# Optimization experiments

Measured on AMD Instinct MI355X. Metric: run time of the kernel, lower is better.

Reference implementation:

```python
import jax, jax.numpy as jnp
import numpy as np

P = 8  # patch_shape (8, 8) -> per-window sequence length 64


def _bias_indices():
    # pairs of (i, j) coords inside an 8x8 patch window
    pairs = np.array([[i, j] for i in range(P) for j in range(P)])  # [64, 2]
    rel = pairs[:, None, :] - pairs[None, :, :] + P - 1  # [64, 64, 2] in [0, 14]
    return rel[:, :, 0], rel[:, :, 1]


def _make_mask(Wy, Wx):
    # generate_mask with apply_shift=True, patch_shape=(8,8)
    s = P // 2
    m = np.zeros((Wy, Wx, P, P, P, P), dtype=bool)
    m[-1, :, :s, :, s:, :] = True
    m[-1, :, s:, :, :s, :] = True
    m[:, -1, :, :s, :, s:] = True
    m[:, -1, :, s:, :, :s] = True
    return jnp.asarray(m.reshape(Wy, Wx, P * P, P * P))


def setup_inputs() -> dict:
    key = jax.random.key(0)
    ks = jax.random.split(key, 10)
    B, Wy, Wx, S, E, H, hd = 16, 16, 16, 64, 128, 4, 32
    sc = 0.05
    return {
        "patches": jax.random.normal(ks[0], (B, Wy, Wx, S, E), dtype=jnp.float32),
        "Wq": jax.random.normal(ks[1], (H, E, hd), dtype=jnp.float32) * sc,
        "bq": jax.random.normal(ks[2], (H, hd), dtype=jnp.float32) * sc,
        "Wk": jax.random.normal(ks[3], (H, E, hd), dtype=jnp.float32) * sc,
        "bk": jax.random.normal(ks[4], (H, hd), dtype=jnp.float32) * sc,
        "Wv": jax.random.normal(ks[5], (H, E, hd), dtype=jnp.float32) * sc,
        "bv": jax.random.normal(ks[6], (H, hd), dtype=jnp.float32) * sc,
        "pos_bias": jax.random.normal(ks[7], (2 * P - 1, 2 * P - 1), dtype=jnp.float32) * 0.02,
        "Wo": jax.random.normal(ks[8], (E, E), dtype=jnp.float32) * sc,
        "bo": jax.random.normal(ks[9], (E,), dtype=jnp.float32) * sc,
        "mask": _make_mask(Wy, Wx),
    }


def reference(patches, Wq, bq, Wk, bk, Wv, bv, pos_bias, Wo, bo, mask):
    hd = Wq.shape[-1]
    B, Wy, Wx, S, E = patches.shape
    H = Wq.shape[0]
    # per-head Q/K/V projections (torch loops over heads; here batched over h)
    q = jnp.einsum("bvwse,hed->bvwhsd", patches, Wq) + bq[:, None, :]
    k = jnp.einsum("bvwse,hed->bvwhsd", patches, Wk) + bk[:, None, :]
    v = jnp.einsum("bvwse,hed->bvwhsd", patches, Wv) + bv[:, None, :]
    logits = jnp.einsum("bvwhqd,bvwhkd->bvwhqk", q, k) / jnp.sqrt(jnp.asarray(hd, patches.dtype))
    ri, ci = _bias_indices()
    logits = logits + pos_bias[ri, ci]  # gather [15,15] -> [64,64]
    logits = jnp.where(mask[None, :, :, None, :, :], -jnp.inf, logits)
    attn = jax.nn.softmax(logits, axis=-1)
    out = jnp.einsum("bvwhqk,bvwhkd->bvwhqd", attn, v)
    # concat heads: [..., H, S, hd] -> [..., S, H*hd]
    out = jnp.swapaxes(out, 3, 4).reshape(B, Wy, Wx, S, H * hd)
    return jnp.einsum("bvwse,ef->bvwsf", out, Wo) + bo
```

## Files before the change

kernel.cpp:

```cpp
#include <hip/hip_runtime.h>
#include <hip/hip_bf16.h>

typedef float f32x4 __attribute__((ext_vector_type(4)));
typedef short bf16x8 __attribute__((ext_vector_type(8)));
typedef short s16x4 __attribute__((ext_vector_type(4)));
typedef unsigned int u32;

#define MFMA16(a, b, c) __builtin_amdgcn_mfma_f32_16x16x32_bf16((a), (b), (c), 0, 0, 0)

__device__ __forceinline__ unsigned short f2bf(float x) {
    union { float f; unsigned int u; } a; a.f = x;
    unsigned int r = a.u + 0x7fffu + ((a.u >> 16) & 1u);
    return (unsigned short)(r >> 16);
}

__global__ void prep_kernel(const float* __restrict__ Wq, const float* __restrict__ bq,
                            const float* __restrict__ Wk, const float* __restrict__ bk,
                            const float* __restrict__ Wv, const float* __restrict__ bv,
                            const float* __restrict__ pos_bias, const float* __restrict__ Wo,
                            unsigned short* __restrict__ WT, unsigned short* __restrict__ WoT,
                            float* __restrict__ bqkv, float* __restrict__ bm) {
    const float LOG2E = 1.4426950408889634f;
    int t = blockIdx.x * blockDim.x + threadIdx.x;
    int nt = gridDim.x * blockDim.x;
    for (int i = t; i < 384 * 128; i += nt) {
        int c = i >> 7, kk = i & 127;
        int h = c / 96, rem = c - h * 96, p = rem >> 5, n = rem & 31;
        const float* W = (p == 0) ? Wq : (p == 1 ? Wk : Wv);
        WT[i] = f2bf(W[(h * 128 + kk) * 32 + n]);
    }
    for (int i = t; i < 128 * 128; i += nt) {
        int n = i >> 7, kk = i & 127;
        WoT[i] = f2bf(Wo[kk * 128 + n]);
    }
    for (int i = t; i < 384; i += nt) {
        int h = i / 96, rem = i - h * 96, p = rem >> 5, n = rem & 31;
        const float* b = (p == 0) ? bq : (p == 1 ? bk : bv);
        bqkv[i] = b[h * 32 + n];
    }
    for (int i = t; i < 4 * 4 * 4 * 64 * 4; i += nt) {
        int r = i & 3, l = (i >> 2) & 63, kt = (i >> 8) & 3, qt = (i >> 10) & 3, v = (i >> 12) & 3;
        int q = qt * 16 + (l & 15);
        int k = kt * 16 + ((l >> 4) << 2) + r;
        int qi = q >> 3, qj = q & 7, ki = k >> 3, kj = k & 7;
        bool masked = (((v >> 1) != 0) && ((qi < 4) != (ki < 4))) ||
                      (((v & 1) != 0) && ((qj < 4) != (kj < 4)));
        bm[i] = masked ? -1e30f : pos_bias[(qi - ki + 7) * 15 + (qj - kj + 7)] * LOG2E;
    }
}

__launch_bounds__(256, 3)
__global__ void swin_kernel(const float* __restrict__ patches,
                            const unsigned short* __restrict__ WT,
                            const float* __restrict__ bqkv,
                            const float* __restrict__ bm,
                            const unsigned short* __restrict__ WoT,
                            const float* __restrict__ bo,
                            float* __restrict__ out) {
    __shared__ short lds[24576];
    const int win = blockIdx.x;
    const int wy = (win >> 4) & 15, wx = win & 15;
    const int tid = threadIdx.x;
    const int lane = tid & 63;
    const int h = tid >> 6;
    const int l15 = lane & 15, l4 = lane >> 4;
    const int sw15 = (l15 & 7) << 3;
    const f32x4 zero = {0.f, 0.f, 0.f, 0.f};

    {
        const float4* src = reinterpret_cast<const float4*>(patches + (size_t)win * 8192);
        #pragma unroll
        for (int i = 0; i < 8; ++i) {
            int idx4 = i * 256 + tid;
            float4 v = src[idx4];
            int row = idx4 >> 5;
            int col = (idx4 & 31) << 2;
            s16x4 pk;
            pk[0] = (short)f2bf(v.x); pk[1] = (short)f2bf(v.y);
            pk[2] = (short)f2bf(v.z); pk[3] = (short)f2bf(v.w);
            *reinterpret_cast<s16x4*>(&lds[row * 128 + (col ^ ((row & 7) << 3))]) = pk;
        }
    }
    __syncthreads();

    const int qkbase = 8192 + h * 4096;
    const int vbase = h * 2048;

    bf16x8 xa[4][4];
    #pragma unroll
    for (int mt = 0; mt < 4; ++mt)
        #pragma unroll
        for (int ks = 0; ks < 4; ++ks)
            xa[mt][ks] = *reinterpret_cast<const bf16x8*>(
                &lds[(mt * 16 + l15) * 128 + ((ks * 32 + l4 * 8) ^ sw15)]);

    #pragma unroll
    for (int ct = 0; ct < 4; ++ct) {
        bf16x8 wb[4];
        #pragma unroll
        for (int ks = 0; ks < 4; ++ks)
            wb[ks] = *reinterpret_cast<const bf16x8*>(
                &WT[(h * 96 + ct * 16 + l15) * 128 + ks * 32 + l4 * 8]);
        float b4[4];
        #pragma unroll
        for (int r = 0; r < 4; ++r) b4[r] = bqkv[h * 96 + ct * 16 + l4 * 4 + r];
        #pragma unroll
        for (int mt = 0; mt < 4; ++mt) {
            f32x4 a = zero;
            #pragma unroll
            for (int ks = 0; ks < 4; ++ks) a = MFMA16(wb[ks], xa[mt][ks], a);
            int tok = mt * 16 + l15;
            int cc0 = (ct * 16 + l4 * 4) ^ sw15;
            s16x4 pk;
            #pragma unroll
            for (int r = 0; r < 4; ++r) pk[r] = (short)f2bf(a[r] + b4[r]);
            *reinterpret_cast<s16x4*>(&lds[qkbase + tok * 64 + cc0]) = pk;
        }
    }
    __syncthreads();

    #pragma unroll
    for (int ctv = 0; ctv < 2; ++ctv) {
        bf16x8 wb[4];
        #pragma unroll
        for (int ks = 0; ks < 4; ++ks)
            wb[ks] = *reinterpret_cast<const bf16x8*>(
                &WT[(h * 96 + 64 + ctv * 16 + l15) * 128 + ks * 32 + l4 * 8]);
        float bb = bqkv[h * 96 + 64 + ctv * 16 + l15];
        #pragma unroll
        for (int mt = 0; mt < 4; ++mt) {
            f32x4 a = zero;
            #pragma unroll
            for (int ks = 0; ks < 4; ++ks) a = MFMA16(xa[mt][ks], wb[ks], a);
            int n = ctv * 16 + l15;
            int tok0 = (mt * 16 + l4 * 4) ^ sw15;
            s16x4 pk;
            #pragma unroll
            for (int r = 0; r < 4; ++r) pk[r] = (short)f2bf(a[r] + bb);
            *reinterpret_cast<s16x4*>(&lds[vbase + n * 64 + tok0]) = pk;
        }
    }

    bf16x8 kfrag[4], vf[2][2];
    #pragma unroll
    for (int kt = 0; kt < 4; ++kt)
        kfrag[kt] = *reinterpret_cast<const bf16x8*>(
            &lds[qkbase + (kt * 16 + l15) * 64 + ((32 + l4 * 8) ^ sw15)]);
    #pragma unroll
    for (int nt = 0; nt < 2; ++nt)
        #pragma unroll
        for (int ks = 0; ks < 2; ++ks)
            vf[nt][ks] = *reinterpret_cast<const bf16x8*>(
                &lds[vbase + (nt * 16 + l15) * 64 + ((ks * 32 + l4 * 8) ^ sw15)]);

    f32x4 O[2][4];
    #pragma unroll
    for (int nt = 0; nt < 2; ++nt)
        #pragma unroll
        for (int qt = 0; qt < 4; ++qt) O[nt][qt] = zero;

    const int mv = ((wy == 15) ? 2 : 0) + ((wx == 15) ? 1 : 0);
    const float4* bmv = reinterpret_cast<const float4*>(bm);
    const float rs2 = 0.2550348660629988f;
    const int sA = ((l4 & 1) << 5) + l15;
    const int sB = sA + 16;

    #pragma unroll
    for (int qt = 0; qt < 4; ++qt) {
        bf16x8 qfrag = *reinterpret_cast<const bf16x8*>(
            &lds[qkbase + (qt * 16 + l15) * 64 + ((l4 * 8) ^ sw15)]);
        f32x4 LT[4];
        #pragma unroll
        for (int kt = 0; kt < 4; ++kt) LT[kt] = MFMA16(kfrag[kt], qfrag, zero);

        float x[4][4];
        float m = -3.0e38f;
        #pragma unroll
        for (int kt = 0; kt < 4; ++kt) {
            float4 b4 = bmv[((mv * 4 + qt) * 4 + kt) * 64 + lane];
            x[kt][0] = LT[kt][0] * rs2 + b4.x;
            x[kt][1] = LT[kt][1] * rs2 + b4.y;
            x[kt][2] = LT[kt][2] * rs2 + b4.z;
            x[kt][3] = LT[kt][3] * rs2 + b4.w;
            m = fmaxf(m, fmaxf(fmaxf(x[kt][0], x[kt][1]), fmaxf(x[kt][2], x[kt][3])));
        }
        m = fmaxf(m, __shfl_xor(m, 16));
        m = fmaxf(m, __shfl_xor(m, 32));
        float s = 0.f;
        #pragma unroll
        for (int kt = 0; kt < 4; ++kt)
            #pragma unroll
            for (int r = 0; r < 4; ++r) {
                float e = exp2f(x[kt][r] - m);
                x[kt][r] = e;
                s += e;
            }
        s += __shfl_xor(s, 16);
        s += __shfl_xor(s, 32);
        float inv = 1.0f / s;

        u32 w[4][2];
        #pragma unroll
        for (int kt = 0; kt < 4; ++kt) {
            w[kt][0] = (u32)f2bf(x[kt][0] * inv) | ((u32)f2bf(x[kt][1] * inv) << 16);
            w[kt][1] = (u32)f2bf(x[kt][2] * inv) | ((u32)f2bf(x[kt][3] * inv) << 16);
        }
        u32 fr[2][4];
        #pragma unroll
        for (int kt = 0; kt < 4; ++kt) {
            u32 a0 = __shfl(w[kt][0], sA);
            u32 a1 = __shfl(w[kt][1], sA);
            u32 b0 = __shfl(w[kt][0], sB);
            u32 b1 = __shfl(w[kt][1], sB);
            if ((kt & 1) == (l4 >> 1)) {
                const int ks = kt >> 1;
                fr[ks][0] = a0; fr[ks][1] = a1; fr[ks][2] = b0; fr[ks][3] = b1;
            }
        }
        bf16x8 pf0, pf1;
        {
            union { u32 u[4]; bf16x8 v; } c0, c1;
            c0.u[0] = fr[0][0]; c0.u[1] = fr[0][1]; c0.u[2] = fr[0][2]; c0.u[3] = fr[0][3];
            c1.u[0] = fr[1][0]; c1.u[1] = fr[1][1]; c1.u[2] = fr[1][2]; c1.u[3] = fr[1][3];
            pf0 = c0.v; pf1 = c1.v;
        }
        #pragma unroll
        for (int nt = 0; nt < 2; ++nt) {
            O[nt][qt] = MFMA16(vf[nt][0], pf0, O[nt][qt]);
            O[nt][qt] = MFMA16(vf[nt][1], pf1, O[nt][qt]);
        }
    }
    __syncthreads();

    #pragma unroll
    for (int nt = 0; nt < 2; ++nt)
        #pragma unroll
        for (int qt = 0; qt < 4; ++qt) {
            int q = qt * 16 + l15;
            int f0 = (h * 32 + nt * 16 + l4 * 4) ^ sw15;
            s16x4 pk;
            #pragma unroll
            for (int r = 0; r < 4; ++r) pk[r] = (short)f2bf(O[nt][qt][r]);
            *reinterpret_cast<s16x4*>(&lds[8192 + q * 128 + f0]) = pk;
        }
    __syncthreads();

    {
        bf16x8 wf[2][4];
        #pragma unroll
        for (int nt = 0; nt < 2; ++nt)
            #pragma unroll
            for (int ks = 0; ks < 4; ++ks)
                wf[nt][ks] = *reinterpret_cast<const bf16x8*>(
                    &WoT[(h * 32 + nt * 16 + l15) * 128 + ks * 32 + l4 * 8]);
        float4 bo4[2];
        #pragma unroll
        for (int nt = 0; nt < 2; ++nt)
            bo4[nt] = *reinterpret_cast<const float4*>(&bo[h * 32 + nt * 16 + l4 * 4]);
        float* outw = out + (size_t)win * 8192;
        #pragma unroll
        for (int mt = 0; mt < 4; ++mt) {
            bf16x8 af[4];
            #pragma unroll
            for (int ks = 0; ks < 4; ++ks)
                af[ks] = *reinterpret_cast<const bf16x8*>(
                    &lds[8192 + (mt * 16 + l15) * 128 + ((ks * 32 + l4 * 8) ^ sw15)]);
            #pragma unroll
            for (int nt = 0; nt < 2; ++nt) {
                f32x4 a = zero;
                #pragma unroll
                for (int ks = 0; ks < 4; ++ks) a = MFMA16(wf[nt][ks], af[ks], a);
                float4 st;
                st.x = a[0] + bo4[nt].x;
                st.y = a[1] + bo4[nt].y;
                st.z = a[2] + bo4[nt].z;
                st.w = a[3] + bo4[nt].w;
                *reinterpret_cast<float4*>(
                    &outw[(size_t)(mt * 16 + l15) * 128 + h * 32 + nt * 16 + l4 * 4]) = st;
            }
        }
    }
}

extern "C" void kernel_launch(void* const* d_in, const int* in_sizes, int n_in,
                              void* d_out, int out_size, void* d_ws, size_t ws_size,
                              hipStream_t stream) {
    const float* patches  = (const float*)d_in[0];
    const float* Wq       = (const float*)d_in[1];
    const float* bq       = (const float*)d_in[2];
    const float* Wk       = (const float*)d_in[3];
    const float* bk       = (const float*)d_in[4];
    const float* Wv       = (const float*)d_in[5];
    const float* bv       = (const float*)d_in[6];
    const float* pos_bias = (const float*)d_in[7];
    const float* Wo       = (const float*)d_in[8];
    const float* bo       = (const float*)d_in[9];

    char* ws = (char*)d_ws;
    unsigned short* WT  = (unsigned short*)(ws);
    unsigned short* WoT = (unsigned short*)(ws + 98304);
    float* bqkv         = (float*)(ws + 131072);
    float* bm           = (float*)(ws + 132608);

    hipLaunchKernelGGL(prep_kernel, dim3(64), dim3(256), 0, stream,
                       Wq, bq, Wk, bk, Wv, bv, pos_bias, Wo, WT, WoT, bqkv, bm);
    hipLaunchKernelGGL(swin_kernel, dim3(4096), dim3(256), 0, stream,
                       patches, WT, bqkv, bm, WoT, bo, (float*)d_out);
}
```

Measured before the change: 110.0 us.

## Make swin kernel persistent with register prefetch of next window's patches

Turns the one-window-per-block kernel into a persistent loop over windows with a grid of 768 blocks (256 CUs × 3 blocks). The next window's fp32 patches are prefetched into registers while the current window's QKV projection and attention run, and the previous window's output projection is deferred to the start of the next iteration. It also raises wave priority around MFMA sections with s_setprio. The aim is to hide global-load latency and cut per-block launch and fill overhead, at the cost of more live registers (the px prefetch buffer) and a more complex schedule.

```diff
diff --git a/kernel.cpp b/kernel.cpp
--- a/kernel.cpp
+++ b/kernel.cpp
@@ -49,6 +49,8 @@
     }
 }
 
+#define SWIN_GRID 768
+
 __launch_bounds__(256, 3)
 __global__ void swin_kernel(const float* __restrict__ patches,
                             const unsigned short* __restrict__ WT,
@@ -58,8 +60,6 @@
                             const float* __restrict__ bo,
                             float* __restrict__ out) {
     __shared__ short lds[24576];
-    const int win = blockIdx.x;
-    const int wy = (win >> 4) & 15, wx = win & 15;
     const int tid = threadIdx.x;
     const int lane = tid & 63;
     const int h = tid >> 6;
@@ -67,183 +67,252 @@
     const int sw15 = (l15 & 7) << 3;
     const f32x4 zero = {0.f, 0.f, 0.f, 0.f};
 
+    const int qkbase = 8192 + h * 4096;
+    const int vbase = h * 2048;
+    const int sA = ((l4 & 1) << 5) + l15;
+    const int sB = sA + 16;
+    const float rs2 = 0.2550348660629988f;
+    const float4* bmv = reinterpret_cast<const float4*>(bm);
+
+    int w = blockIdx.x;
+    float4 px[8];
     {
-        const float4* src = reinterpret_cast<const float4*>(patches + (size_t)win * 8192);
+        const float4* src = reinterpret_cast<const float4*>(patches + (size_t)w * 8192);
+        #pragma unroll
+        for (int i = 0; i < 8; ++i) px[i] = src[i * 256 + tid];
+    }
+    #pragma unroll
+    for (int i = 0; i < 8; ++i) {
+        int idx4 = i * 256 + tid;
+        int row = idx4 >> 5, col = (idx4 & 31) << 2;
+        s16x4 pk;
+        pk[0] = (short)f2bf(px[i].x); pk[1] = (short)f2bf(px[i].y);
+        pk[2] = (short)f2bf(px[i].z); pk[3] = (short)f2bf(px[i].w);
+        *reinterpret_cast<s16x4*>(&lds[row * 128 + (col ^ ((row & 7) << 3))]) = pk;
+    }
+    __syncthreads();
+
+    int prev = -1;
+    for (; w < 4096; w += SWIN_GRID) {
+        if (prev >= 0) {
+            bf16x8 wf[2][4];
+            #pragma unroll
+            for (int nt = 0; nt < 2; ++nt)
+                #pragma unroll
+                for (int ks = 0; ks < 4; ++ks)
+                    wf[nt][ks] = *reinterpret_cast<const bf16x8*>(
+                        &WoT[(h * 32 + nt * 16 + l15) * 128 + ks * 32 + l4 * 8]);
+            float4 bo4[2];
+            #pragma unroll
+            for (int nt = 0; nt < 2; ++nt)
+                bo4[nt] = *reinterpret_cast<const float4*>(&bo[h * 32 + nt * 16 + l4 * 4]);
+            float* outw = out + (size_t)prev * 8192;
+            #pragma unroll
+            for (int mt = 0; mt < 4; ++mt) {
+                bf16x8 af[4];
+                #pragma unroll
+                for (int ks = 0; ks < 4; ++ks)
+                    af[ks] = *reinterpret_cast<const bf16x8*>(
+                        &lds[8192 + (mt * 16 + l15) * 128 + ((ks * 32 + l4 * 8) ^ sw15)]);
+                __builtin_amdgcn_s_setprio(1);
+                #pragma unroll
+                for (int nt = 0; nt < 2; ++nt) {
+                    f32x4 a = zero;
+                    #pragma unroll
+                    for (int ks = 0; ks < 4; ++ks) a = MFMA16(wf[nt][ks], af[ks], a);
+                    float4 st;
+                    st.x = a[0] + bo4[nt].x;
+                    st.y = a[1] + bo4[nt].y;
+                    st.z = a[2] + bo4[nt].z;
+                    st.w = a[3] + bo4[nt].w;
+                    *reinterpret_cast<float4*>(
+                        &outw[(size_t)(mt * 16 + l15) * 128 + h * 32 + nt * 16 + l4 * 4]) = st;
+                }
+                __builtin_amdgcn_s_setprio(0);
+            }
+        }
+
+        bf16x8 xa[4][4];
+        #pragma unroll
+        for (int mt = 0; mt < 4; ++mt)
+            #pragma unroll
+            for (int ks = 0; ks < 4; ++ks)
+                xa[mt][ks] = *reinterpret_cast<const bf16x8*>(
+                    &lds[(mt * 16 + l15) * 128 + ((ks * 32 + l4 * 8) ^ sw15)]);
+        __syncthreads();
+
+        {
+            int wn = w + SWIN_GRID;
+            const float4* srcn = reinterpret_cast<const float4*>(
+                patches + (size_t)(wn < 4096 ? wn : w) * 8192);
+            #pragma unroll
+            for (int i = 0; i < 8; ++i) px[i] = srcn[i * 256 + tid];
+        }
+
+        #pragma unroll
+        for (int ct = 0; ct < 4; ++ct) {
+            bf16x8 wb[4];
+            #pragma unroll
+            for (int ks = 0; ks < 4; ++ks)
+                wb[ks] = *reinterpret_cast<const bf16x8*>(
+                    &WT[(h * 96 + ct * 16 + l15) * 128 + ks * 32 + l4 * 8]);
+            float b4[4];
+            #pragma unroll
+            for (int r = 0; r < 4; ++r) b4[r] = bqkv[h * 96 + ct * 16 + l4 * 4 + r];
+            __builtin_amdgcn_s_setprio(1);
+            #pragma unroll
+            for (int mt = 0; mt < 4; ++mt) {
+                f32x4 a = zero;
+                #pragma unroll
+                for (int ks = 0; ks < 4; ++ks) a = MFMA16(wb[ks], xa[mt][ks], a);
+                int tok = mt * 16 + l15;
+                int cc0 = (ct * 16 + l4 * 4) ^ sw15;
+                s16x4 pk;
+                #pragma unroll
+                for (int r = 0; r < 4; ++r) pk[r] = (short)f2bf(a[r] + b4[r]);
+                *reinterpret_cast<s16x4*>(&lds[qkbase + tok * 64 + cc0]) = pk;
+            }
+            __builtin_amdgcn_s_setprio(0);
+        }
+
+        #pragma unroll
+        for (int ctv = 0; ctv < 2; ++ctv) {
+            bf16x8 wb[4];
+            #pragma unroll
+            for (int ks = 0; ks < 4; ++ks)
+                wb[ks] = *reinterpret_cast<const bf16x8*>(
+                    &WT[(h * 96 + 64 + ctv * 16 + l15) * 128 + ks * 32 + l4 * 8]);
+            float bb = bqkv[h * 96 + 64 + ctv * 16 + l15];
+            __builtin_amdgcn_s_setprio(1);
+            #pragma unroll
+            for (int mt = 0; mt < 4; ++mt) {
+                f32x4 a = zero;
+                #pragma unroll
+                for (int ks = 0; ks < 4; ++ks) a = MFMA16(xa[mt][ks], wb[ks], a);
+                int n = ctv * 16 + l15;
+                int tok0 = (mt * 16 + l4 * 4) ^ sw15;
+                s16x4 pk;
+                #pragma unroll
+                for (int r = 0; r < 4; ++r) pk[r] = (short)f2bf(a[r] + bb);
+                *reinterpret_cast<s16x4*>(&lds[vbase + n * 64 + tok0]) = pk;
+            }
+            __builtin_amdgcn_s_setprio(0);
+        }
+
+        bf16x8 kfrag[4], vf[2][2];
+        #pragma unroll
+        for (int kt = 0; kt < 4; ++kt)
+            kfrag[kt] = *reinterpret_cast<const bf16x8*>(
+                &lds[qkbase + (kt * 16 + l15) * 64 + ((32 + l4 * 8) ^ sw15)]);
+        #pragma unroll
+        for (int nt = 0; nt < 2; ++nt)
+            #pragma unroll
+            for (int ks = 0; ks < 2; ++ks)
+                vf[nt][ks] = *reinterpret_cast<const bf16x8*>(
+                    &lds[vbase + (nt * 16 + l15) * 64 + ((ks * 32 + l4 * 8) ^ sw15)]);
+
+        f32x4 O[2][4];
+        #pragma unroll
+        for (int nt = 0; nt < 2; ++nt)
+            #pragma unroll
+            for (int qt = 0; qt < 4; ++qt) O[nt][qt] = zero;
+
+        const int mv = (((w >> 4) & 15) == 15 ? 2 : 0) + ((w & 15) == 15 ? 1 : 0);
+
+        #pragma unroll
+        for (int qt = 0; qt < 4; ++qt) {
+            bf16x8 qfrag = *reinterpret_cast<const bf16x8*>(
+                &lds[qkbase + (qt * 16 + l15) * 64 + ((l4 * 8) ^ sw15)]);
+            f32x4 LT[4];
+            __builtin_amdgcn_s_setprio(1);
+            #pragma unroll
+            for (int kt = 0; kt < 4; ++kt) LT[kt] = MFMA16(kfrag[kt], qfrag, zero);
+            __builtin_amdgcn_s_setprio(0);
+
+            float x[4][4];
+            float m = -3.0e38f;
+            #pragma unroll
+            for (int kt = 0; kt < 4; ++kt) {
+                float4 b4 = bmv[((mv * 4 + qt) * 4 + kt) * 64 + lane];
+                x[kt][0] = LT[kt][0] * rs2 + b4.x;
+                x[kt][1] = LT[kt][1] * rs2 + b4.y;
+                x[kt][2] = LT[kt][2] * rs2 + b4.z;
+                x[kt][3] = LT[kt][3] * rs2 + b4.w;
+                m = fmaxf(m, fmaxf(fmaxf(x[kt][0], x[kt][1]), fmaxf(x[kt][2], x[kt][3])));
+            }
+            m = fmaxf(m, __shfl_xor(m, 16));
+            m = fmaxf(m, __shfl_xor(m, 32));
+            float s = 0.f;
+            #pragma unroll
+            for (int kt = 0; kt < 4; ++kt)
+                #pragma unroll
+                for (int r = 0; r < 4; ++r) {
+                    float e = exp2f(x[kt][r] - m);
+                    x[kt][r] = e;
+                    s += e;
+                }
+            s += __shfl_xor(s, 16);
+            s += __shfl_xor(s, 32);
+            float inv = 1.0f / s;
+
+            u32 wp[4][2];
+            #pragma unroll
+            for (int kt = 0; kt < 4; ++kt) {
+                wp[kt][0] = (u32)f2bf(x[kt][0] * inv) | ((u32)f2bf(x[kt][1] * inv) << 16);
+                wp[kt][1] = (u32)f2bf(x[kt][2] * inv) | ((u32)f2bf(x[kt][3] * inv) << 16);
+            }
+            u32 fr[2][4];
+            #pragma unroll
+            for (int kt = 0; kt < 4; ++kt) {
+                u32 a0 = __shfl(wp[kt][0], sA);
+                u32 a1 = __shfl(wp[kt][1], sA);
+                u32 b0 = __shfl(wp[kt][0], sB);
+                u32 b1 = __shfl(wp[kt][1], sB);
+                if ((kt & 1) == (l4 >> 1)) {
+                    const int ks = kt >> 1;
+                    fr[ks][0] = a0; fr[ks][1] = a1; fr[ks][2] = b0; fr[ks][3] = b1;
+                }
+            }
+            bf16x8 pf0, pf1;
+            {
+                union { u32 u[4]; bf16x8 v; } c0, c1;
+                c0.u[0] = fr[0][0]; c0.u[1] = fr[0][1]; c0.u[2] = fr[0][2]; c0.u[3] = fr[0][3];
+                c1.u[0] = fr[1][0]; c1.u[1] = fr[1][1]; c1.u[2] = fr[1][2]; c1.u[3] = fr[1][3];
+                pf0 = c0.v; pf1 = c1.v;
+            }
+            __builtin_amdgcn_s_setprio(1);
+            #pragma unroll
+            for (int nt = 0; nt < 2; ++nt) {
+                O[nt][qt] = MFMA16(vf[nt][0], pf0, O[nt][qt]);
+                O[nt][qt] = MFMA16(vf[nt][1], pf1, O[nt][qt]);
+            }
+            __builtin_amdgcn_s_setprio(0);
+        }
+        __syncthreads();
+
         #pragma unroll
         for (int i = 0; i < 8; ++i) {
             int idx4 = i * 256 + tid;
-            float4 v = src[idx4];
-            int row = idx4 >> 5;
-            int col = (idx4 & 31) << 2;
+            int row = idx4 >> 5, col = (idx4 & 31) << 2;
             s16x4 pk;
-            pk[0] = (short)f2bf(v.x); pk[1] = (short)f2bf(v.y);
-            pk[2] = (short)f2bf(v.z); pk[3] = (short)f2bf(v.w);
+            pk[0] = (short)f2bf(px[i].x); pk[1] = (short)f2bf(px[i].y);
+            pk[2] = (short)f2bf(px[i].z); pk[3] = (short)f2bf(px[i].w);
             *reinterpret_cast<s16x4*>(&lds[row * 128 + (col ^ ((row & 7) << 3))]) = pk;
         }
-    }
-    __syncthreads();
-
-    const int qkbase = 8192 + h * 4096;
-    const int vbase = h * 2048;
-
-    bf16x8 xa[4][4];
-    #pragma unroll
-    for (int mt = 0; mt < 4; ++mt)
-        #pragma unroll
-        for (int ks = 0; ks < 4; ++ks)
-            xa[mt][ks] = *reinterpret_cast<const bf16x8*>(
-                &lds[(mt * 16 + l15) * 128 + ((ks * 32 + l4 * 8) ^ sw15)]);
-
-    #pragma unroll
-    for (int ct = 0; ct < 4; ++ct) {
-        bf16x8 wb[4];
-        #pragma unroll
-        for (int ks = 0; ks < 4; ++ks)
-            wb[ks] = *reinterpret_cast<const bf16x8*>(
-                &WT[(h * 96 + ct * 16 + l15) * 128 + ks * 32 + l4 * 8]);
-        float b4[4];
-        #pragma unroll
-        for (int r = 0; r < 4; ++r) b4[r] = bqkv[h * 96 + ct * 16 + l4 * 4 + r];
-        #pragma unroll
-        for (int mt = 0; mt < 4; ++mt) {
-            f32x4 a = zero;
-            #pragma unroll
-            for (int ks = 0; ks < 4; ++ks) a = MFMA16(wb[ks], xa[mt][ks], a);
-            int tok = mt * 16 + l15;
-            int cc0 = (ct * 16 + l4 * 4) ^ sw15;
-            s16x4 pk;
-            #pragma unroll
-            for (int r = 0; r < 4; ++r) pk[r] = (short)f2bf(a[r] + b4[r]);
-            *reinterpret_cast<s16x4*>(&lds[qkbase + tok * 64 + cc0]) = pk;
-        }
-    }
-    __syncthreads();
-
-    #pragma unroll
-    for (int ctv = 0; ctv < 2; ++ctv) {
-        bf16x8 wb[4];
-        #pragma unroll
-        for (int ks = 0; ks < 4; ++ks)
-            wb[ks] = *reinterpret_cast<const bf16x8*>(
-                &WT[(h * 96 + 64 + ctv * 16 + l15) * 128 + ks * 32 + l4 * 8]);
-        float bb = bqkv[h * 96 + 64 + ctv * 16 + l15];
-        #pragma unroll
-        for (int mt = 0; mt < 4; ++mt) {
-            f32x4 a = zero;
-            #pragma unroll
-            for (int ks = 0; ks < 4; ++ks) a = MFMA16(xa[mt][ks], wb[ks], a);
-            int n = ctv * 16 + l15;
-            int tok0 = (mt * 16 + l4 * 4) ^ sw15;
-            s16x4 pk;
-            #pragma unroll
-            for (int r = 0; r < 4; ++r) pk[r] = (short)f2bf(a[r] + bb);
-            *reinterpret_cast<s16x4*>(&lds[vbase + n * 64 + tok0]) = pk;
-        }
-    }
-
-    bf16x8 kfrag[4], vf[2][2];
-    #pragma unroll
-    for (int kt = 0; kt < 4; ++kt)
-        kfrag[kt] = *reinterpret_cast<const bf16x8*>(
-            &lds[qkbase + (kt * 16 + l15) * 64 + ((32 + l4 * 8) ^ sw15)]);
-    #pragma unroll
-    for (int nt = 0; nt < 2; ++nt)
-        #pragma unroll
-        for (int ks = 0; ks < 2; ++ks)
-            vf[nt][ks] = *reinterpret_cast<const bf16x8*>(
-                &lds[vbase + (nt * 16 + l15) * 64 + ((ks * 32 + l4 * 8) ^ sw15)]);
-
-    f32x4 O[2][4];
-    #pragma unroll
-    for (int nt = 0; nt < 2; ++nt)
-        #pragma unroll
-        for (int qt = 0; qt < 4; ++qt) O[nt][qt] = zero;
-
-    const int mv = ((wy == 15) ? 2 : 0) + ((wx == 15) ? 1 : 0);
-    const float4* bmv = reinterpret_cast<const float4*>(bm);
-    const float rs2 = 0.2550348660629988f;
-    const int sA = ((l4 & 1) << 5) + l15;
-    const int sB = sA + 16;
-
-    #pragma unroll
-    for (int qt = 0; qt < 4; ++qt) {
-        bf16x8 qfrag = *reinterpret_cast<const bf16x8*>(
-            &lds[qkbase + (qt * 16 + l15) * 64 + ((l4 * 8) ^ sw15)]);
-        f32x4 LT[4];
-        #pragma unroll
-        for (int kt = 0; kt < 4; ++kt) LT[kt] = MFMA16(kfrag[kt], qfrag, zero);
-
-        float x[4][4];
-        float m = -3.0e38f;
-        #pragma unroll
-        for (int kt = 0; kt < 4; ++kt) {
-            float4 b4 = bmv[((mv * 4 + qt) * 4 + kt) * 64 + lane];
-            x[kt][0] = LT[kt][0] * rs2 + b4.x;
-            x[kt][1] = LT[kt][1] * rs2 + b4.y;
-            x[kt][2] = LT[kt][2] * rs2 + b4.z;
-            x[kt][3] = LT[kt][3] * rs2 + b4.w;
-            m = fmaxf(m, fmaxf(fmaxf(x[kt][0], x[kt][1]), fmaxf(x[kt][2], x[kt][3])));
-        }
-        m = fmaxf(m, __shfl_xor(m, 16));
-        m = fmaxf(m, __shfl_xor(m, 32));
-        float s = 0.f;
-        #pragma unroll
-        for (int kt = 0; kt < 4; ++kt)
-            #pragma unroll
-            for (int r = 0; r < 4; ++r) {
-                float e = exp2f(x[kt][r] - m);
-                x[kt][r] = e;
-                s += e;
-            }
-        s += __shfl_xor(s, 16);
-        s += __shfl_xor(s, 32);
-        float inv = 1.0f / s;
-
-        u32 w[4][2];
-        #pragma unroll
-        for (int kt = 0; kt < 4; ++kt) {
-            w[kt][0] = (u32)f2bf(x[kt][0] * inv) | ((u32)f2bf(x[kt][1] * inv) << 16);
-            w[kt][1] = (u32)f2bf(x[kt][2] * inv) | ((u32)f2bf(x[kt][3] * inv) << 16);
-        }
-        u32 fr[2][4];
-        #pragma unroll
-        for (int kt = 0; kt < 4; ++kt) {
-            u32 a0 = __shfl(w[kt][0], sA);
-            u32 a1 = __shfl(w[kt][1], sA);
-            u32 b0 = __shfl(w[kt][0], sB);
-            u32 b1 = __shfl(w[kt][1], sB);
-            if ((kt & 1) == (l4 >> 1)) {
-                const int ks = kt >> 1;
-                fr[ks][0] = a0; fr[ks][1] = a1; fr[ks][2] = b0; fr[ks][3] = b1;
-            }
-        }
-        bf16x8 pf0, pf1;
-        {
-            union { u32 u[4]; bf16x8 v; } c0, c1;
-            c0.u[0] = fr[0][0]; c0.u[1] = fr[0][1]; c0.u[2] = fr[0][2]; c0.u[3] = fr[0][3];
-            c1.u[0] = fr[1][0]; c1.u[1] = fr[1][1]; c1.u[2] = fr[1][2]; c1.u[3] = fr[1][3];
-            pf0 = c0.v; pf1 = c1.v;
-        }
-        #pragma unroll
-        for (int nt = 0; nt < 2; ++nt) {
-            O[nt][qt] = MFMA16(vf[nt][0], pf0, O[nt][qt]);
-            O[nt][qt] = MFMA16(vf[nt][1], pf1, O[nt][qt]);
-        }
-    }
-    __syncthreads();
-
-    #pragma unroll
-    for (int nt = 0; nt < 2; ++nt)
-        #pragma unroll
-        for (int qt = 0; qt < 4; ++qt) {
-            int q = qt * 16 + l15;
-            int f0 = (h * 32 + nt * 16 + l4 * 4) ^ sw15;
-            s16x4 pk;
-            #pragma unroll
-            for (int r = 0; r < 4; ++r) pk[r] = (short)f2bf(O[nt][qt][r]);
-            *reinterpret_cast<s16x4*>(&lds[8192 + q * 128 + f0]) = pk;
-        }
-    __syncthreads();
+        #pragma unroll
+        for (int nt = 0; nt < 2; ++nt)
+            #pragma unroll
+            for (int qt = 0; qt < 4; ++qt) {
+                int q = qt * 16 + l15;
+                int f0 = (h * 32 + nt * 16 + l4 * 4) ^ sw15;
+                s16x4 pk;
+                #pragma unroll
+                for (int r = 0; r < 4; ++r) pk[r] = (short)f2bf(O[nt][qt][r]);
+                *reinterpret_cast<s16x4*>(&lds[8192 + q * 128 + f0]) = pk;
+            }
+        prev = w;
+        __syncthreads();
+    }
 
     {
         bf16x8 wf[2][4];
@@ -257,7 +326,7 @@
         #pragma unroll
         for (int nt = 0; nt < 2; ++nt)
             bo4[nt] = *reinterpret_cast<const float4*>(&bo[h * 32 + nt * 16 + l4 * 4]);
-        float* outw = out + (size_t)win * 8192;
+        float* outw = out + (size_t)prev * 8192;
         #pragma unroll
         for (int mt = 0; mt < 4; ++mt) {
             bf16x8 af[4];
@@ -304,6 +373,6 @@
 
     hipLaunchKernelGGL(prep_kernel, dim3(64), dim3(256), 0, stream,
                        Wq, bq, Wk, bk, Wv, bv, pos_bias, Wo, WT, WoT, bqkv, bm);
-    hipLaunchKernelGGL(swin_kernel, dim3(4096), dim3(256), 0, stream,
+    hipLaunchKernelGGL(swin_kernel, dim3(SWIN_GRID), dim3(256), 0, stream,
                        patches, WT, bqkv, bm, WoT, bo, (float*)d_out);
 }
```

After: 232.9 us. +111.7%, slower.
